# Performance work log

Hardware: AMD Instinct MI355X
Metric: run time of the kernel (lower is better)

## Reference

```python
import jax, jax.numpy as jnp
import numpy as np

B, S, D, H, DFF = 4, 2048, 1024, 8, 4096
DH = D // H  # 128
EPS = 1e-5


def layernorm(x, gamma, beta):
    mu = jnp.mean(x, axis=-1, keepdims=True)
    var = jnp.mean(jnp.square(x - mu), axis=-1, keepdims=True)
    return (x - mu) * jax.lax.rsqrt(var + EPS) * gamma + beta


def setup_inputs() -> dict:
    key = jax.random.key(0)
    ks = jax.random.split(key, 6)
    s = 0.02
    return {
        "src": jax.random.normal(ks[0], (B, S, D), jnp.float32),
        "w_qkv": jax.random.normal(ks[1], (D, 3 * D), jnp.float32) * s,
        "w_out": jax.random.normal(ks[2], (D, D), jnp.float32) * s,
        "w1": jax.random.normal(ks[3], (D, DFF), jnp.float32) * s,
        "b1": jnp.zeros((DFF,), jnp.float32),
        "w2": jax.random.normal(ks[4], (DFF, D), jnp.float32) * s,
        "b2": jnp.zeros((D,), jnp.float32),
        "g1": jnp.ones((D,), jnp.float32),
        "beta1": jnp.zeros((D,), jnp.float32),
        "g2": jnp.ones((D,), jnp.float32),
        "beta2": jnp.zeros((D,), jnp.float32),
    }


def reference(src, w_qkv, w_out, w1, b1, w2, b2, g1, beta1, g2, beta2):
    b, s, d = src.shape
    # --- RingAttention == exact causal MHA on a single device ---
    qkv = src @ w_qkv  # [b, s, 3d]
    q, k, v = jnp.split(qkv, 3, axis=-1)
    to_heads = lambda x: x.reshape(b, s, H, DH).transpose(0, 2, 1, 3)  # [b,h,s,dh]
    q, k, v = to_heads(q), to_heads(k), to_heads(v)
    scale = 1.0 / jnp.sqrt(jnp.asarray(DH, src.dtype))
    scores = jnp.einsum('bhqd,bhkd->bhqk', q, k) * scale  # [b,h,s,s]
    causal = jnp.tril(jnp.ones((s, s), bool))
    neg = jnp.asarray(jnp.finfo(src.dtype).min, src.dtype)
    scores = jnp.where(causal, scores, neg)
    attn = jax.nn.softmax(scores, axis=-1)
    o = jnp.einsum('bhqk,bhkd->bhqd', attn, v)  # [b,h,s,dh]
    o = o.transpose(0, 2, 1, 3).reshape(b, s, d) @ w_out
    # dropout layers are identity at inference
    x = layernorm(src + o, g1, beta1)
    ff = jax.nn.relu(x @ w1 + b1) @ w2 + b2
    return layernorm(x + ff, g2, beta2)
```

## Files before the change

kernel.cpp:

```cpp
#include <hip/hip_runtime.h>

typedef unsigned short u16;
typedef __attribute__((ext_vector_type(8))) short short8;
typedef __attribute__((ext_vector_type(4))) float float4v;

#define MFMA_BF16(a, b, c) __builtin_amdgcn_mfma_f32_16x16x32_bf16((a), (b), (c), 0, 0, 0)

#define B_ 4
#define S_ 2048
#define D_ 1024
#define H_ 8
#define DH_ 128
#define DFF_ 4096
#define EPS_ 1e-5f
#define ROWS_ (B_ * S_)
#define CSCALE_ 0.12751672939502f

__device__ __forceinline__ u16 f2bf(float f) {
  union { float f; unsigned u; } x; x.f = f;
  unsigned r = x.u + 0x7fffu + ((x.u >> 16) & 1u);
  return (u16)(r >> 16);
}

typedef __attribute__((address_space(1))) const unsigned int guint;
typedef __attribute__((address_space(3))) unsigned int luint;
__device__ __forceinline__ void gl2lds16(const u16* g, u16* l) {
  __builtin_amdgcn_global_load_lds((guint*)g, (luint*)l, 16, 0, 0);
}

__global__ void cast_bf16_kernel(const float* __restrict__ in, u16* __restrict__ out, int n4) {
  int i = blockIdx.x * blockDim.x + threadIdx.x;
  int stride = gridDim.x * blockDim.x;
  for (; i < n4; i += stride) {
    float4 v = ((const float4*)in)[i];
    ushort4 u;
    u.x = f2bf(v.x); u.y = f2bf(v.y); u.z = f2bf(v.z); u.w = f2bf(v.w);
    ((ushort4*)out)[i] = u;
  }
}

__global__ void transpose_cast_kernel(const float* __restrict__ in, u16* __restrict__ out,
                                      int K, int N) {
  __shared__ float t[32][33];
  int k0 = blockIdx.x * 32, n0 = blockIdx.y * 32;
  int tx = threadIdx.x & 31, ty = threadIdx.x >> 5;
  #pragma unroll
  for (int i = 0; i < 4; ++i)
    t[ty + 8 * i][tx] = in[(size_t)(k0 + ty + 8 * i) * N + n0 + tx];
  __syncthreads();
  #pragma unroll
  for (int i = 0; i < 4; ++i)
    out[(size_t)(n0 + ty + 8 * i) * K + k0 + tx] = f2bf(t[tx][ty + 8 * i]);
}

__global__ void transpose_v_kernel(const u16* __restrict__ in, u16* __restrict__ out) {
  __shared__ u16 t[32][33];
  int s0 = blockIdx.x * 32, d0 = blockIdx.y * 32, bh = blockIdx.z;
  const u16* src = in + (size_t)bh * S_ * DH_;
  u16* dst = out + (size_t)bh * DH_ * S_;
  int tx = threadIdx.x & 31, ty = threadIdx.x >> 5;
  #pragma unroll
  for (int i = 0; i < 4; ++i)
    t[ty + 8 * i][tx] = src[(size_t)(s0 + ty + 8 * i) * DH_ + d0 + tx];
  __syncthreads();
  #pragma unroll
  for (int i = 0; i < 4; ++i)
    dst[(size_t)(d0 + ty + 8 * i) * S_ + s0 + tx] = t[tx][ty + 8 * i];
}

template <int MODE>
__global__ __launch_bounds__(512, 2) void gemm256_kernel(
    const u16* __restrict__ A, const u16* __restrict__ Bt,
    const int M, const int N, const int K,
    float* __restrict__ outF, u16* __restrict__ outH, const float* __restrict__ bias,
    u16* __restrict__ qo, u16* __restrict__ ko, u16* __restrict__ vo) {
  extern __shared__ u16 smem[];
  u16* At  = smem;
  u16* Bts = smem + 2 * 256 * 64;
  const int tid = threadIdx.x;
  const int lane = tid & 63, wave = tid >> 6;
  const int quad = lane >> 4, r16 = lane & 15;
  const int halfw = wave >> 2;
  const int wn = (wave & 3) * 64;
  const int m0 = blockIdx.x * 256, n0 = blockIdx.y * 256;
  const int NT = K >> 6;

  const int rowin = wave * 8 + (lane >> 3);
  const int sc = lane & 7;
  const int shalf = rowin >> 5, srr = rowin & 31;

  const u16* Asrc[4];
  const u16* Bsrc[4];
  #pragma unroll
  for (int u = 0; u < 4; ++u) {
    const int ra = shalf * 128 + u * 32 + srr;
    Asrc[u] = A + (size_t)(m0 + ra) * K + (sc ^ (ra & 7)) * 8;
    const int rb = u * 64 + rowin;
    Bsrc[u] = Bt + (size_t)(n0 + rb) * K + (sc ^ (rb & 7)) * 8;
  }

  float4v acc[8][4];
  #pragma unroll
  for (int i = 0; i < 8; ++i)
    #pragma unroll
    for (int j = 0; j < 4; ++j) acc[i][j] = (float4v)0.0f;

#define STAGE_A(t, u) gl2lds16(Asrc[u] + (t) * 64, At  + ((t) & 1) * 16384 + (u) * 4096 + wave * 512)
#define STAGE_B(t, u) gl2lds16(Bsrc[u] + (t) * 64, Bts + ((t) & 1) * 16384 + (u) * 4096 + wave * 512)

  STAGE_B(0, 0); STAGE_B(0, 1); STAGE_B(0, 2); STAGE_B(0, 3);
  STAGE_A(0, 0); STAGE_A(0, 1); STAGE_A(0, 2); STAGE_A(0, 3);
  if (NT > 1) {
    STAGE_B(1, 0); STAGE_B(1, 1); STAGE_B(1, 2); STAGE_B(1, 3);
    STAGE_A(1, 0); STAGE_A(1, 1);
    asm volatile("s_waitcnt vmcnt(6)" ::: "memory");
  } else {
    asm volatile("s_waitcnt vmcnt(0)" ::: "memory");
  }
  __builtin_amdgcn_s_barrier();

  for (int kt = 0; kt < NT; ++kt) {
    const u16* Ab = At + (kt & 1) * 16384;
    const u16* Bb = Bts + (kt & 1) * 16384;
    short8 bfr[4][2];
    #pragma unroll
    for (int q = 0; q < 4; ++q) {
      if (q == 0) {
        #pragma unroll
        for (int j = 0; j < 4; ++j)
          #pragma unroll
          for (int s = 0; s < 2; ++s)
            bfr[j][s] = *(const short8*)(Bb + (wn + j * 16 + r16) * 64 +
                                         (((s * 4 + quad) ^ (r16 & 7)) * 8));
      }
      short8 af[2][2];
      #pragma unroll
      for (int di = 0; di < 2; ++di)
        #pragma unroll
        for (int s = 0; s < 2; ++s)
          af[di][s] = *(const short8*)(Ab + (q * 64 + halfw * 32 + di * 16 + r16) * 64 +
                                       (((s * 4 + quad) ^ (r16 & 7)) * 8));
      if (q == 0)      { if (kt + 1 < NT) { STAGE_A(kt + 1, 2); STAGE_A(kt + 1, 3); } }
      else if (q == 1) { if (kt + 2 < NT) { STAGE_B(kt + 2, 0); STAGE_B(kt + 2, 1); } }
      else if (q == 2) { if (kt + 2 < NT) { STAGE_B(kt + 2, 2); STAGE_B(kt + 2, 3); } }
      else             { if (kt + 2 < NT) { STAGE_A(kt + 2, 0); STAGE_A(kt + 2, 1); } }
      __builtin_amdgcn_s_barrier();
      asm volatile("s_waitcnt lgkmcnt(0)" ::: "memory");
      __builtin_amdgcn_s_setprio(1);
      #pragma unroll
      for (int j = 0; j < 4; ++j) {
        acc[2 * q][j]     = MFMA_BF16(af[0][0], bfr[j][0], acc[2 * q][j]);
        acc[2 * q][j]     = MFMA_BF16(af[0][1], bfr[j][1], acc[2 * q][j]);
        acc[2 * q + 1][j] = MFMA_BF16(af[1][0], bfr[j][0], acc[2 * q + 1][j]);
        acc[2 * q + 1][j] = MFMA_BF16(af[1][1], bfr[j][1], acc[2 * q + 1][j]);
      }
      __builtin_amdgcn_s_setprio(0);
      if (q == 3) {
        if (kt + 2 < NT)      { asm volatile("s_waitcnt vmcnt(6)" ::: "memory"); }
        else if (kt + 1 < NT) { asm volatile("s_waitcnt vmcnt(0)" ::: "memory"); }
      }
      __builtin_amdgcn_s_barrier();
    }
  }
#undef STAGE_A
#undef STAGE_B

  #pragma unroll
  for (int i = 0; i < 8; ++i) {
    const int rowb = m0 + halfw * 128 + i * 16 + quad * 4;
    #pragma unroll
    for (int j = 0; j < 4; ++j) {
      const int col = n0 + wn + j * 16 + r16;
      #pragma unroll
      for (int rg = 0; rg < 4; ++rg) {
        float val = acc[i][j][rg];
        const int r = rowb + rg;
        if (MODE == 2) {
          val += bias[col];
          val = fmaxf(val, 0.0f);
          outH[(size_t)r * N + col] = f2bf(val);
        } else {
          outF[(size_t)r * N + col] = val;
        }
      }
    }
  }
}

template <int MODE>
__global__ __launch_bounds__(512, 2) void gemm256x128_kernel(
    const u16* __restrict__ A, const u16* __restrict__ Bt,
    const int M, const int N, const int K,
    float* __restrict__ outF, u16* __restrict__ outH, const float* __restrict__ bias,
    u16* __restrict__ qo, u16* __restrict__ ko, u16* __restrict__ vo) {
  extern __shared__ u16 smem[];
  u16* At  = smem;
  u16* Bts = smem + 2 * 256 * 64;
  const int tid = threadIdx.x;
  const int lane = tid & 63, wave = tid >> 6;
  const int quad = lane >> 4, r16 = lane & 15;
  const int w64 = wave >> 1;
  const int wn = (wave & 1) * 64;
  const int m0 = blockIdx.x * 256, n0 = blockIdx.y * 128;
  const int NT = K >> 6;

  const int rowin = wave * 8 + (lane >> 3);
  const int sc = lane & 7;

  const u16* Asrc[4];
  const u16* Bsrc[2];
  #pragma unroll
  for (int u = 0; u < 4; ++u) {
    const int ra = ((u & 1) * 2 + (rowin >> 5)) * 64 + (u >> 1) * 32 + (rowin & 31);
    Asrc[u] = A + (size_t)(m0 + ra) * K + (sc ^ (ra & 7)) * 8;
  }
  #pragma unroll
  for (int u = 0; u < 2; ++u) {
    const int rb = u * 64 + rowin;
    Bsrc[u] = Bt + (size_t)(n0 + rb) * K + (sc ^ (rb & 7)) * 8;
  }

  float4v acc[4][4];
  #pragma unroll
  for (int i = 0; i < 4; ++i)
    #pragma unroll
    for (int j = 0; j < 4; ++j) acc[i][j] = (float4v)0.0f;

#define STAGE_A(t, u) gl2lds16(Asrc[u] + (t) * 64, At  + ((t) & 1) * 16384 + (u) * 4096 + wave * 512)
#define STAGE_B(t, u) gl2lds16(Bsrc[u] + (t) * 64, Bts + ((t) & 1) * 8192 + (u) * 4096 + wave * 512)

  STAGE_B(0, 0); STAGE_B(0, 1); STAGE_A(0, 0); STAGE_A(0, 1);
  STAGE_A(0, 2); STAGE_A(0, 3);
  STAGE_B(1, 0); STAGE_B(1, 1); STAGE_A(1, 0); STAGE_A(1, 1);
  asm volatile("s_waitcnt vmcnt(6)" ::: "memory");
  __builtin_amdgcn_s_barrier();

  for (int kt = 0; kt < NT; ++kt) {
    const u16* Ab = At + (kt & 1) * 16384;
    const u16* Bb = Bts + (kt & 1) * 8192;
    short8 bfr[4][2];
    #pragma unroll
    for (int j = 0; j < 4; ++j)
      #pragma unroll
      for (int s = 0; s < 2; ++s)
        bfr[j][s] = *(const short8*)(Bb + (wn + j * 16 + r16) * 64 +
                                     (((s * 4 + quad) ^ (r16 & 7)) * 8));
    {
      short8 af[2][2];
      #pragma unroll
      for (int di = 0; di < 2; ++di)
        #pragma unroll
        for (int s = 0; s < 2; ++s)
          af[di][s] = *(const short8*)(Ab + (w64 * 32 + di * 16 + r16) * 64 +
                                       (((s * 4 + quad) ^ (r16 & 7)) * 8));
      if (kt + 1 < NT) { STAGE_A(kt + 1, 2); STAGE_A(kt + 1, 3); }
      __builtin_amdgcn_s_barrier();
      asm volatile("s_waitcnt lgkmcnt(0)" ::: "memory");
      __builtin_amdgcn_s_setprio(1);
      #pragma unroll
      for (int j = 0; j < 4; ++j) {
        acc[0][j] = MFMA_BF16(af[0][0], bfr[j][0], acc[0][j]);
        acc[0][j] = MFMA_BF16(af[0][1], bfr[j][1], acc[0][j]);
        acc[1][j] = MFMA_BF16(af[1][0], bfr[j][0], acc[1][j]);
        acc[1][j] = MFMA_BF16(af[1][1], bfr[j][1], acc[1][j]);
      }
      __builtin_amdgcn_s_setprio(0);
      if (kt + 1 < NT) { asm volatile("s_waitcnt vmcnt(6)" ::: "memory"); }
      else             { asm volatile("s_waitcnt vmcnt(0)" ::: "memory"); }
      __builtin_amdgcn_s_barrier();
    }
    {
      short8 af[2][2];
      #pragma unroll
      for (int di = 0; di < 2; ++di)
        #pragma unroll
        for (int s = 0; s < 2; ++s)
          af[di][s] = *(const short8*)(Ab + (128 + w64 * 32 + di * 16 + r16) * 64 +
                                       (((s * 4 + quad) ^ (r16 & 7)) * 8));
      if (kt + 2 < NT) {
        STAGE_B(kt + 2, 0); STAGE_B(kt + 2, 1);
        STAGE_A(kt + 2, 0); STAGE_A(kt + 2, 1);
      }
      __builtin_amdgcn_s_barrier();
      asm volatile("s_waitcnt lgkmcnt(0)" ::: "memory");
      __builtin_amdgcn_s_setprio(1);
      #pragma unroll
      for (int j = 0; j < 4; ++j) {
        acc[2][j] = MFMA_BF16(af[0][0], bfr[j][0], acc[2][j]);
        acc[2][j] = MFMA_BF16(af[0][1], bfr[j][1], acc[2][j]);
        acc[3][j] = MFMA_BF16(af[1][0], bfr[j][0], acc[3][j]);
        acc[3][j] = MFMA_BF16(af[1][1], bfr[j][1], acc[3][j]);
      }
      __builtin_amdgcn_s_setprio(0);
      if (kt + 1 < NT) {
        if (kt + 2 < NT) { asm volatile("s_waitcnt vmcnt(6)" ::: "memory"); }
        else             { asm volatile("s_waitcnt vmcnt(2)" ::: "memory"); }
      }
      __builtin_amdgcn_s_barrier();
    }
  }
#undef STAGE_A
#undef STAGE_B

  #pragma unroll
  for (int i = 0; i < 4; ++i) {
    const int rowb = m0 + w64 * 64 + i * 16 + quad * 4;
    #pragma unroll
    for (int j = 0; j < 4; ++j) {
      const int col = n0 + wn + j * 16 + r16;
      #pragma unroll
      for (int rg = 0; rg < 4; ++rg) {
        float val = acc[i][j][rg];
        const int r = rowb + rg;
        if (MODE == 0) {
          const int part = col >> 10, cc = col & 1023;
          const int h = cc >> 7, dh = cc & 127;
          const int b = r >> 11, s = r & 2047;
          u16* dst = (part == 0) ? qo : (part == 1) ? ko : vo;
          if (part == 0) val *= CSCALE_;
          dst[((size_t)(b * H_ + h) * S_ + s) * DH_ + dh] = f2bf(val);
        } else if (MODE == 1) {
          outF[(size_t)r * N + col] = val;
        } else {
          val += bias[col];
          outF[(size_t)r * N + col] = val;
        }
      }
    }
  }
}

__global__ __launch_bounds__(256) void attn_kernel(
    const u16* __restrict__ Q, const u16* __restrict__ Kg,
    const u16* __restrict__ Vtg, u16* __restrict__ O) {
  __shared__ u16 Ks[64][136];
  __shared__ u16 Vt[128][72];
  __shared__ u16 Pw[4][16][72];
  const int tid = threadIdx.x;
  const int lane = tid & 63, wave = tid >> 6;
  const int quad = lane >> 4, r16 = lane & 15;
  const int id = blockIdx.x;
  const int bh = (id & 7) * 4 + (id >> 7);
  const int pairIdx = (id >> 3) & 15;
  const size_t base = (size_t)bh * S_ * DH_;
  const size_t vtb = (size_t)bh * DH_ * S_;
  const int b = bh >> 3, h = bh & 7;

  const u16* kg0 = Kg + base + (size_t)(tid >> 4) * DH_ + (tid & 15) * 8;
  u16* ksl = &Ks[tid >> 4][(tid & 15) * 8];
  const u16* vg0 = Vtg + vtb + (size_t)(tid >> 3) * S_ + (tid & 7) * 8;
  u16* vtl = &Vt[tid >> 3][(tid & 7) * 8];

  short8 rk[4], rv[4];
#define LOADKV(kb_)                                                        \
  do {                                                                     \
    _Pragma("unroll")                                                      \
    for (int i_ = 0; i_ < 4; ++i_)                                         \
      rk[i_] = *(const short8*)(kg0 + (size_t)((kb_) * 64 + i_ * 16) * DH_); \
    _Pragma("unroll")                                                      \
    for (int i_ = 0; i_ < 4; ++i_)                                         \
      rv[i_] = *(const short8*)(vg0 + (size_t)i_ * 32 * S_ + (kb_) * 64);  \
  } while (0)

  for (int half = 0; half < 2; ++half) {
    const int qb = (half == 0) ? pairIdx : 31 - pairIdx;
    const int qr = qb * 64 + wave * 16 + r16;

    short8 aq[4];
    #pragma unroll
    for (int ks = 0; ks < 4; ++ks)
      aq[ks] = *(const short8*)(Q + base + (size_t)qr * DH_ + ks * 32 + quad * 8);

    float4v acco[8];
    #pragma unroll
    for (int i = 0; i < 8; ++i) acco[i] = (float4v)0.0f;
    float m_q = -1e30f, l_q = 0.0f;

    LOADKV(0);

    for (int kb = 0; kb <= qb; ++kb) {
      __syncthreads();
      #pragma unroll
      for (int i = 0; i < 4; ++i) *(short8*)(ksl + i * 16 * 136) = rk[i];
      #pragma unroll
      for (int i = 0; i < 4; ++i) *(short8*)(vtl + i * 32 * 72) = rv[i];
      __syncthreads();
      if (kb < qb) LOADKV(kb + 1);

      float4v accs[4];
      #pragma unroll
      for (int t = 0; t < 4; ++t) accs[t] = (float4v)0.0f;
      #pragma unroll
      for (int ks = 0; ks < 4; ++ks) {
        #pragma unroll
        for (int t = 0; t < 4; ++t) {
          short8 ak = *(const short8*)&Ks[t * 16 + r16][ks * 32 + quad * 8];
          accs[t] = MFMA_BF16(ak, aq[ks], accs[t]);
        }
      }
      if (kb == qb) {
        #pragma unroll
        for (int t = 0; t < 4; ++t)
          #pragma unroll
          for (int rg = 0; rg < 4; ++rg) {
            int kc = kb * 64 + t * 16 + quad * 4 + rg;
            if (kc > qr) accs[t][rg] = -1e30f;
          }
      }
      float mv = accs[0][0];
      #pragma unroll
      for (int t = 0; t < 4; ++t)
        #pragma unroll
        for (int rg = 0; rg < 4; ++rg) mv = fmaxf(mv, accs[t][rg]);
      mv = fmaxf(mv, __shfl_xor(mv, 16));
      mv = fmaxf(mv, __shfl_xor(mv, 32));
      const float mnew = fmaxf(m_q, mv);
      const float alpha = __builtin_amdgcn_exp2f(m_q - mnew);
      float s0 = 0.0f;
      #pragma unroll
      for (int t = 0; t < 4; ++t)
        #pragma unroll
        for (int rg = 0; rg < 4; ++rg) {
          float p = __builtin_amdgcn_exp2f(accs[t][rg] - mnew);
          accs[t][rg] = p;
          s0 += p;
        }
      s0 += __shfl_xor(s0, 16);
      s0 += __shfl_xor(s0, 32);
      l_q = l_q * alpha + s0;
      m_q = mnew;

      #pragma unroll
      for (int t = 0; t < 4; ++t) {
        union { float f; unsigned u; } c0, c1, c2, c3;
        c0.f = accs[t][0]; c1.f = accs[t][1]; c2.f = accs[t][2]; c3.f = accs[t][3];
        uint2 pk;
        pk.x = ((c0.u + 0x8000u) >> 16) | ((c1.u + 0x8000u) & 0xffff0000u);
        pk.y = ((c2.u + 0x8000u) >> 16) | ((c3.u + 0x8000u) & 0xffff0000u);
        *(uint2*)&Pw[wave][r16][t * 16 + quad * 4] = pk;
      }
      float al[4];
      #pragma unroll
      for (int rg = 0; rg < 4; ++rg) al[rg] = __shfl(alpha, quad * 4 + rg);
      #pragma unroll
      for (int nt = 0; nt < 8; ++nt)
        #pragma unroll
        for (int rg = 0; rg < 4; ++rg) acco[nt][rg] *= al[rg];
      asm volatile("s_waitcnt lgkmcnt(0)" ::: "memory");
      #pragma unroll
      for (int ks2 = 0; ks2 < 2; ++ks2) {
        short8 ap = *(const short8*)&Pw[wave][r16][ks2 * 32 + quad * 8];
        #pragma unroll
        for (int nt = 0; nt < 8; ++nt) {
          short8 bv = *(const short8*)&Vt[nt * 16 + r16][ks2 * 32 + quad * 8];
          acco[nt] = MFMA_BF16(ap, bv, acco[nt]);
        }
      }
    }

    float lr[4];
    #pragma unroll
    for (int rg = 0; rg < 4; ++rg) lr[rg] = __shfl(l_q, quad * 4 + rg);
    const int sbase = qb * 64 + wave * 16 + quad * 4;
    #pragma unroll
    for (int nt = 0; nt < 8; ++nt)
      #pragma unroll
      for (int rg = 0; rg < 4; ++rg) {
        float val = acco[nt][rg] / lr[rg];
        O[((size_t)(b * S_ + sbase + rg)) * D_ + h * DH_ + nt * 16 + r16] = f2bf(val);
      }
  }
#undef LOADKV
}

__global__ __launch_bounds__(256) void ln_kernel(
    const float* __restrict__ a, const float* __restrict__ res,
    const float* __restrict__ g, const float* __restrict__ be,
    float* __restrict__ xf, u16* __restrict__ xb) {
  __shared__ float red[8];
  const int row = blockIdx.x, tid = threadIdx.x;
  const float4 va = ((const float4*)(a + (size_t)row * D_))[tid];
  const float4 vr = ((const float4*)(res + (size_t)row * D_))[tid];
  float4 v;
  v.x = va.x + vr.x; v.y = va.y + vr.y; v.z = va.z + vr.z; v.w = va.w + vr.w;
  float s = v.x + v.y + v.z + v.w;
  float q = v.x * v.x + v.y * v.y + v.z * v.z + v.w * v.w;
  #pragma unroll
  for (int m = 1; m < 64; m <<= 1) {
    s += __shfl_xor(s, m);
    q += __shfl_xor(q, m);
  }
  const int wave = tid >> 6, lane = tid & 63;
  if (lane == 0) { red[wave] = s; red[4 + wave] = q; }
  __syncthreads();
  s = red[0] + red[1] + red[2] + red[3];
  q = red[4] + red[5] + red[6] + red[7];
  const float mu = s * (1.0f / D_);
  const float var = q * (1.0f / D_) - mu * mu;
  const float inv = rsqrtf(var + EPS_);
  const float4 gg = ((const float4*)g)[tid];
  const float4 bb = ((const float4*)be)[tid];
  float4 y;
  y.x = (v.x - mu) * inv * gg.x + bb.x;
  y.y = (v.y - mu) * inv * gg.y + bb.y;
  y.z = (v.z - mu) * inv * gg.z + bb.z;
  y.w = (v.w - mu) * inv * gg.w + bb.w;
  ((float4*)(xf + (size_t)row * D_))[tid] = y;
  if (xb) {
    ushort4 u;
    u.x = f2bf(y.x); u.y = f2bf(y.y); u.z = f2bf(y.z); u.w = f2bf(y.w);
    ((ushort4*)(xb + (size_t)row * D_))[tid] = u;
  }
}

extern "C" void kernel_launch(void* const* d_in, const int* in_sizes, int n_in,
                              void* d_out, int out_size, void* d_ws, size_t ws_size,
                              hipStream_t stream) {
  const float* src   = (const float*)d_in[0];
  const float* w_qkv = (const float*)d_in[1];
  const float* w_out = (const float*)d_in[2];
  const float* w1    = (const float*)d_in[3];
  const float* b1    = (const float*)d_in[4];
  const float* w2    = (const float*)d_in[5];
  const float* b2    = (const float*)d_in[6];
  const float* g1    = (const float*)d_in[7];
  const float* be1   = (const float*)d_in[8];
  const float* g2    = (const float*)d_in[9];
  const float* be2   = (const float*)d_in[10];
  float* out = (float*)d_out;

  char* ws = (char*)d_ws;
  size_t off = 0;
  auto alloc = [&](size_t bytes) -> void* {
    void* p = ws + off;
    off += (bytes + 255) & ~(size_t)255;
    return p;
  };
  u16* src_bf = (u16*)alloc((size_t)ROWS_ * D_ * 2);
  u16* wqkvT  = (u16*)alloc((size_t)3 * D_ * D_ * 2);
  u16* woutT  = (u16*)alloc((size_t)D_ * D_ * 2);
  u16* w1T    = (u16*)alloc((size_t)DFF_ * D_ * 2);
  u16* w2T    = (u16*)alloc((size_t)D_ * DFF_ * 2);
  u16* qbuf   = (u16*)alloc((size_t)ROWS_ * D_ * 2);
  u16* kbuf   = (u16*)alloc((size_t)ROWS_ * D_ * 2);
  u16* vbuf   = (u16*)alloc((size_t)ROWS_ * D_ * 2);
  u16* obuf   = (u16*)alloc((size_t)ROWS_ * D_ * 2);
  u16* vT     = (u16*)alloc((size_t)ROWS_ * D_ * 2);
  float* proj = (float*)alloc((size_t)ROWS_ * D_ * 4);
  float* xf   = (float*)alloc((size_t)ROWS_ * D_ * 4);
  u16* xb     = (u16*)alloc((size_t)ROWS_ * D_ * 2);
  u16* h1     = qbuf;
  float* ff   = proj;

  const int GSMEM  = 131072;
  const int GSMEM2 = 98304;
  hipFuncSetAttribute((const void*)gemm256_kernel<2>, hipFuncAttributeMaxDynamicSharedMemorySize, GSMEM);
  hipFuncSetAttribute((const void*)gemm256x128_kernel<0>, hipFuncAttributeMaxDynamicSharedMemorySize, GSMEM2);
  hipFuncSetAttribute((const void*)gemm256x128_kernel<1>, hipFuncAttributeMaxDynamicSharedMemorySize, GSMEM2);
  hipFuncSetAttribute((const void*)gemm256x128_kernel<3>, hipFuncAttributeMaxDynamicSharedMemorySize, GSMEM2);

  cast_bf16_kernel<<<2048, 256, 0, stream>>>(src, src_bf, ROWS_ * D_ / 4);
  transpose_cast_kernel<<<dim3(D_ / 32, 3 * D_ / 32), 256, 0, stream>>>(w_qkv, wqkvT, D_, 3 * D_);
  transpose_cast_kernel<<<dim3(D_ / 32, D_ / 32), 256, 0, stream>>>(w_out, woutT, D_, D_);
  transpose_cast_kernel<<<dim3(D_ / 32, DFF_ / 32), 256, 0, stream>>>(w1, w1T, D_, DFF_);
  transpose_cast_kernel<<<dim3(DFF_ / 32, D_ / 32), 256, 0, stream>>>(w2, w2T, DFF_, D_);

  gemm256x128_kernel<0><<<dim3(ROWS_ / 256, 3 * D_ / 128), 512, GSMEM2, stream>>>(
      src_bf, wqkvT, ROWS_, 3 * D_, D_, nullptr, nullptr, nullptr, qbuf, kbuf, vbuf);
  transpose_v_kernel<<<dim3(S_ / 32, DH_ / 32, B_ * H_), 256, 0, stream>>>(vbuf, vT);
  attn_kernel<<<512, 256, 0, stream>>>(qbuf, kbuf, vT, obuf);
  gemm256x128_kernel<1><<<dim3(ROWS_ / 256, D_ / 128), 512, GSMEM2, stream>>>(
      obuf, woutT, ROWS_, D_, D_, proj, nullptr, nullptr, nullptr, nullptr, nullptr);
  ln_kernel<<<ROWS_, 256, 0, stream>>>(proj, src, g1, be1, xf, xb);
  gemm256_kernel<2><<<dim3(ROWS_ / 256, DFF_ / 256), 512, GSMEM, stream>>>(
      xb, w1T, ROWS_, DFF_, D_, nullptr, h1, b1, nullptr, nullptr, nullptr);
  gemm256x128_kernel<3><<<dim3(ROWS_ / 256, D_ / 128), 512, GSMEM2, stream>>>(
      h1, w2T, ROWS_, D_, DFF_, ff, nullptr, b2, nullptr, nullptr, nullptr);
  ln_kernel<<<ROWS_, 256, 0, stream>>>(ff, xf, g2, be2, out, nullptr);
}
```

Measured before the change: 481.3 us.

## Split-K the second FFN GEMM, unpair attention blocks, add lazy softmax rescaling

The FFN down-projection GEMM is split into two K halves across blockIdx.z. Each half writes its own fp32 partial, and the second LayerNorm sums the two partials, which raises block count for the long-K GEMM. The attention kernel drops the paired causal-block scheme and launches one block per query tile (1024 blocks), heaviest tiles first. The online softmax skips the output rescale when the running max grows by less than a threshold. The split adds an extra fp32 buffer write and read, and ff2 is placed at the start of ws, which may overlap other buffers.

```diff
diff --git a/kernel.cpp b/kernel.cpp
--- a/kernel.cpp
+++ b/kernel.cpp
@@ -190,8 +190,9 @@
 template <int MODE>
 __global__ __launch_bounds__(512, 2) void gemm256x128_kernel(
     const u16* __restrict__ A, const u16* __restrict__ Bt,
-    const int M, const int N, const int K,
-    float* __restrict__ outF, u16* __restrict__ outH, const float* __restrict__ bias,
+    const int M, const int N, const int K, const int lda,
+    float* __restrict__ outF, float* __restrict__ outF2,
+    u16* __restrict__ outH, const float* __restrict__ bias,
     u16* __restrict__ qo, u16* __restrict__ ko, u16* __restrict__ vo) {
   extern __shared__ u16 smem[];
   u16* At  = smem;
@@ -203,6 +204,7 @@
   const int wn = (wave & 1) * 64;
   const int m0 = blockIdx.x * 256, n0 = blockIdx.y * 128;
   const int NT = K >> 6;
+  const int kof = (MODE == 4) ? (int)blockIdx.z * K : 0;
 
   const int rowin = wave * 8 + (lane >> 3);
   const int sc = lane & 7;
@@ -212,12 +214,12 @@
   #pragma unroll
   for (int u = 0; u < 4; ++u) {
     const int ra = ((u & 1) * 2 + (rowin >> 5)) * 64 + (u >> 1) * 32 + (rowin & 31);
-    Asrc[u] = A + (size_t)(m0 + ra) * K + (sc ^ (ra & 7)) * 8;
+    Asrc[u] = A + (size_t)(m0 + ra) * lda + kof + (sc ^ (ra & 7)) * 8;
   }
   #pragma unroll
   for (int u = 0; u < 2; ++u) {
     const int rb = u * 64 + rowin;
-    Bsrc[u] = Bt + (size_t)(n0 + rb) * K + (sc ^ (rb & 7)) * 8;
+    Bsrc[u] = Bt + (size_t)(n0 + rb) * lda + kof + (sc ^ (rb & 7)) * 8;
   }
 
   float4v acc[4][4];
@@ -321,6 +323,10 @@
           dst[((size_t)(b * H_ + h) * S_ + s) * DH_ + dh] = f2bf(val);
         } else if (MODE == 1) {
           outF[(size_t)r * N + col] = val;
+        } else if (MODE == 4) {
+          float* dst = blockIdx.z ? outF2 : outF;
+          if (blockIdx.z == 0) val += bias[col];
+          dst[(size_t)r * N + col] = val;
         } else {
           val += bias[col];
           outF[(size_t)r * N + col] = val;
@@ -340,8 +346,8 @@
   const int lane = tid & 63, wave = tid >> 6;
   const int quad = lane >> 4, r16 = lane & 15;
   const int id = blockIdx.x;
-  const int bh = (id & 7) * 4 + (id >> 7);
-  const int pairIdx = (id >> 3) & 15;
+  const int bh = (id & 7) * 4 + ((id >> 3) & 3);
+  const int qb = 31 - (id >> 5);
   const size_t base = (size_t)bh * S_ * DH_;
   const size_t vtb = (size_t)bh * DH_ * S_;
   const int b = bh >> 3, h = bh & 7;
@@ -362,83 +368,84 @@
       rv[i_] = *(const short8*)(vg0 + (size_t)i_ * 32 * S_ + (kb_) * 64);  \
   } while (0)
 
-  for (int half = 0; half < 2; ++half) {
-    const int qb = (half == 0) ? pairIdx : 31 - pairIdx;
-    const int qr = qb * 64 + wave * 16 + r16;
-
-    short8 aq[4];
-    #pragma unroll
-    for (int ks = 0; ks < 4; ++ks)
-      aq[ks] = *(const short8*)(Q + base + (size_t)qr * DH_ + ks * 32 + quad * 8);
-
-    float4v acco[8];
-    #pragma unroll
-    for (int i = 0; i < 8; ++i) acco[i] = (float4v)0.0f;
-    float m_q = -1e30f, l_q = 0.0f;
-
-    LOADKV(0);
-
-    for (int kb = 0; kb <= qb; ++kb) {
-      __syncthreads();
-      #pragma unroll
-      for (int i = 0; i < 4; ++i) *(short8*)(ksl + i * 16 * 136) = rk[i];
-      #pragma unroll
-      for (int i = 0; i < 4; ++i) *(short8*)(vtl + i * 32 * 72) = rv[i];
-      __syncthreads();
-      if (kb < qb) LOADKV(kb + 1);
-
-      float4v accs[4];
-      #pragma unroll
-      for (int t = 0; t < 4; ++t) accs[t] = (float4v)0.0f;
-      #pragma unroll
-      for (int ks = 0; ks < 4; ++ks) {
-        #pragma unroll
-        for (int t = 0; t < 4; ++t) {
-          short8 ak = *(const short8*)&Ks[t * 16 + r16][ks * 32 + quad * 8];
-          accs[t] = MFMA_BF16(ak, aq[ks], accs[t]);
-        }
-      }
-      if (kb == qb) {
-        #pragma unroll
-        for (int t = 0; t < 4; ++t)
-          #pragma unroll
-          for (int rg = 0; rg < 4; ++rg) {
-            int kc = kb * 64 + t * 16 + quad * 4 + rg;
-            if (kc > qr) accs[t][rg] = -1e30f;
-          }
-      }
-      float mv = accs[0][0];
-      #pragma unroll
-      for (int t = 0; t < 4; ++t)
-        #pragma unroll
-        for (int rg = 0; rg < 4; ++rg) mv = fmaxf(mv, accs[t][rg]);
-      mv = fmaxf(mv, __shfl_xor(mv, 16));
-      mv = fmaxf(mv, __shfl_xor(mv, 32));
-      const float mnew = fmaxf(m_q, mv);
-      const float alpha = __builtin_amdgcn_exp2f(m_q - mnew);
-      float s0 = 0.0f;
+  const int qr = qb * 64 + wave * 16 + r16;
+
+  short8 aq[4];
+  #pragma unroll
+  for (int ks = 0; ks < 4; ++ks)
+    aq[ks] = *(const short8*)(Q + base + (size_t)qr * DH_ + ks * 32 + quad * 8);
+
+  float4v acco[8];
+  #pragma unroll
+  for (int i = 0; i < 8; ++i) acco[i] = (float4v)0.0f;
+  float m_q = -1e30f, l_q = 0.0f;
+
+  LOADKV(0);
+
+  for (int kb = 0; kb <= qb; ++kb) {
+    __syncthreads();
+    #pragma unroll
+    for (int i = 0; i < 4; ++i) *(short8*)(ksl + i * 16 * 136) = rk[i];
+    #pragma unroll
+    for (int i = 0; i < 4; ++i) *(short8*)(vtl + i * 32 * 72) = rv[i];
+    __syncthreads();
+    if (kb < qb) LOADKV(kb + 1);
+
+    float4v accs[4];
+    #pragma unroll
+    for (int t = 0; t < 4; ++t) accs[t] = (float4v)0.0f;
+    #pragma unroll
+    for (int ks = 0; ks < 4; ++ks) {
+      #pragma unroll
+      for (int t = 0; t < 4; ++t) {
+        short8 ak = *(const short8*)&Ks[t * 16 + r16][ks * 32 + quad * 8];
+        accs[t] = MFMA_BF16(ak, aq[ks], accs[t]);
+      }
+    }
+    if (kb == qb) {
       #pragma unroll
       for (int t = 0; t < 4; ++t)
         #pragma unroll
         for (int rg = 0; rg < 4; ++rg) {
-          float p = __builtin_amdgcn_exp2f(accs[t][rg] - mnew);
-          accs[t][rg] = p;
-          s0 += p;
+          int kc = kb * 64 + t * 16 + quad * 4 + rg;
+          if (kc > qr) accs[t][rg] = -1e30f;
         }
-      s0 += __shfl_xor(s0, 16);
-      s0 += __shfl_xor(s0, 32);
-      l_q = l_q * alpha + s0;
-      m_q = mnew;
-
-      #pragma unroll
-      for (int t = 0; t < 4; ++t) {
-        union { float f; unsigned u; } c0, c1, c2, c3;
-        c0.f = accs[t][0]; c1.f = accs[t][1]; c2.f = accs[t][2]; c3.f = accs[t][3];
-        uint2 pk;
-        pk.x = ((c0.u + 0x8000u) >> 16) | ((c1.u + 0x8000u) & 0xffff0000u);
-        pk.y = ((c2.u + 0x8000u) >> 16) | ((c3.u + 0x8000u) & 0xffff0000u);
-        *(uint2*)&Pw[wave][r16][t * 16 + quad * 4] = pk;
-      }
+    }
+    float mv = accs[0][0];
+    #pragma unroll
+    for (int t = 0; t < 4; ++t)
+      #pragma unroll
+      for (int rg = 0; rg < 4; ++rg) mv = fmaxf(mv, accs[t][rg]);
+    mv = fmaxf(mv, __shfl_xor(mv, 16));
+    mv = fmaxf(mv, __shfl_xor(mv, 32));
+    const bool nore = __all(mv <= m_q + 8.0f) != 0;
+    const float mnew = nore ? m_q : fmaxf(m_q, mv);
+    float alpha = 1.0f;
+    if (!nore) alpha = __builtin_amdgcn_exp2f(m_q - mnew);
+    float s0 = 0.0f;
+    #pragma unroll
+    for (int t = 0; t < 4; ++t)
+      #pragma unroll
+      for (int rg = 0; rg < 4; ++rg) {
+        float p = __builtin_amdgcn_exp2f(accs[t][rg] - mnew);
+        accs[t][rg] = p;
+        s0 += p;
+      }
+    s0 += __shfl_xor(s0, 16);
+    s0 += __shfl_xor(s0, 32);
+    l_q = nore ? (l_q + s0) : (l_q * alpha + s0);
+    m_q = mnew;
+
+    #pragma unroll
+    for (int t = 0; t < 4; ++t) {
+      union { float f; unsigned u; } c0, c1, c2, c3;
+      c0.f = accs[t][0]; c1.f = accs[t][1]; c2.f = accs[t][2]; c3.f = accs[t][3];
+      uint2 pk;
+      pk.x = ((c0.u + 0x8000u) >> 16) | ((c1.u + 0x8000u) & 0xffff0000u);
+      pk.y = ((c2.u + 0x8000u) >> 16) | ((c3.u + 0x8000u) & 0xffff0000u);
+      *(uint2*)&Pw[wave][r16][t * 16 + quad * 4] = pk;
+    }
+    if (!nore) {
       float al[4];
       #pragma unroll
       for (int rg = 0; rg < 4; ++rg) al[rg] = __shfl(alpha, quad * 4 + rg);
@@ -446,35 +453,36 @@
       for (int nt = 0; nt < 8; ++nt)
         #pragma unroll
         for (int rg = 0; rg < 4; ++rg) acco[nt][rg] *= al[rg];
-      asm volatile("s_waitcnt lgkmcnt(0)" ::: "memory");
-      #pragma unroll
-      for (int ks2 = 0; ks2 < 2; ++ks2) {
-        short8 ap = *(const short8*)&Pw[wave][r16][ks2 * 32 + quad * 8];
-        #pragma unroll
-        for (int nt = 0; nt < 8; ++nt) {
-          short8 bv = *(const short8*)&Vt[nt * 16 + r16][ks2 * 32 + quad * 8];
-          acco[nt] = MFMA_BF16(ap, bv, acco[nt]);
-        }
-      }
-    }
-
-    float lr[4];
-    #pragma unroll
-    for (int rg = 0; rg < 4; ++rg) lr[rg] = __shfl(l_q, quad * 4 + rg);
-    const int sbase = qb * 64 + wave * 16 + quad * 4;
-    #pragma unroll
-    for (int nt = 0; nt < 8; ++nt)
-      #pragma unroll
-      for (int rg = 0; rg < 4; ++rg) {
-        float val = acco[nt][rg] / lr[rg];
-        O[((size_t)(b * S_ + sbase + rg)) * D_ + h * DH_ + nt * 16 + r16] = f2bf(val);
-      }
-  }
+    }
+    asm volatile("s_waitcnt lgkmcnt(0)" ::: "memory");
+    #pragma unroll
+    for (int ks2 = 0; ks2 < 2; ++ks2) {
+      short8 ap = *(const short8*)&Pw[wave][r16][ks2 * 32 + quad * 8];
+      #pragma unroll
+      for (int nt = 0; nt < 8; ++nt) {
+        short8 bv = *(const short8*)&Vt[nt * 16 + r16][ks2 * 32 + quad * 8];
+        acco[nt] = MFMA_BF16(ap, bv, acco[nt]);
+      }
+    }
+  }
+
+  float lr[4];
+  #pragma unroll
+  for (int rg = 0; rg < 4; ++rg) lr[rg] = __shfl(l_q, quad * 4 + rg);
+  const int sbase = qb * 64 + wave * 16 + quad * 4;
+  #pragma unroll
+  for (int nt = 0; nt < 8; ++nt)
+    #pragma unroll
+    for (int rg = 0; rg < 4; ++rg) {
+      float val = acco[nt][rg] / lr[rg];
+      O[((size_t)(b * S_ + sbase + rg)) * D_ + h * DH_ + nt * 16 + r16] = f2bf(val);
+    }
 #undef LOADKV
 }
 
 __global__ __launch_bounds__(256) void ln_kernel(
-    const float* __restrict__ a, const float* __restrict__ res,
+    const float* __restrict__ a, const float* __restrict__ a2,
+    const float* __restrict__ res,
     const float* __restrict__ g, const float* __restrict__ be,
     float* __restrict__ xf, u16* __restrict__ xb) {
   __shared__ float red[8];
@@ -483,6 +491,10 @@
   const float4 vr = ((const float4*)(res + (size_t)row * D_))[tid];
   float4 v;
   v.x = va.x + vr.x; v.y = va.y + vr.y; v.z = va.z + vr.z; v.w = va.w + vr.w;
+  if (a2) {
+    const float4 v2 = ((const float4*)(a2 + (size_t)row * D_))[tid];
+    v.x += v2.x; v.y += v2.y; v.z += v2.z; v.w += v2.w;
+  }
   float s = v.x + v.y + v.z + v.w;
   float q = v.x * v.x + v.y * v.y + v.z * v.z + v.w * v.w;
   #pragma unroll
@@ -551,13 +563,14 @@
   u16* xb     = (u16*)alloc((size_t)ROWS_ * D_ * 2);
   u16* h1     = qbuf;
   float* ff   = proj;
+  float* ff2  = (float*)ws;
 
   const int GSMEM  = 131072;
   const int GSMEM2 = 98304;
   hipFuncSetAttribute((const void*)gemm256_kernel<2>, hipFuncAttributeMaxDynamicSharedMemorySize, GSMEM);
   hipFuncSetAttribute((const void*)gemm256x128_kernel<0>, hipFuncAttributeMaxDynamicSharedMemorySize, GSMEM2);
   hipFuncSetAttribute((const void*)gemm256x128_kernel<1>, hipFuncAttributeMaxDynamicSharedMemorySize, GSMEM2);
-  hipFuncSetAttribute((const void*)gemm256x128_kernel<3>, hipFuncAttributeMaxDynamicSharedMemorySize, GSMEM2);
+  hipFuncSetAttribute((const void*)gemm256x128_kernel<4>, hipFuncAttributeMaxDynamicSharedMemorySize, GSMEM2);
 
   cast_bf16_kernel<<<2048, 256, 0, stream>>>(src, src_bf, ROWS_ * D_ / 4);
   transpose_cast_kernel<<<dim3(D_ / 32, 3 * D_ / 32), 256, 0, stream>>>(w_qkv, wqkvT, D_, 3 * D_);
@@ -566,15 +579,15 @@
   transpose_cast_kernel<<<dim3(DFF_ / 32, D_ / 32), 256, 0, stream>>>(w2, w2T, DFF_, D_);
 
   gemm256x128_kernel<0><<<dim3(ROWS_ / 256, 3 * D_ / 128), 512, GSMEM2, stream>>>(
-      src_bf, wqkvT, ROWS_, 3 * D_, D_, nullptr, nullptr, nullptr, qbuf, kbuf, vbuf);
+      src_bf, wqkvT, ROWS_, 3 * D_, D_, D_, nullptr, nullptr, nullptr, nullptr, qbuf, kbuf, vbuf);
   transpose_v_kernel<<<dim3(S_ / 32, DH_ / 32, B_ * H_), 256, 0, stream>>>(vbuf, vT);
-  attn_kernel<<<512, 256, 0, stream>>>(qbuf, kbuf, vT, obuf);
+  attn_kernel<<<1024, 256, 0, stream>>>(qbuf, kbuf, vT, obuf);
   gemm256x128_kernel<1><<<dim3(ROWS_ / 256, D_ / 128), 512, GSMEM2, stream>>>(
-      obuf, woutT, ROWS_, D_, D_, proj, nullptr, nullptr, nullptr, nullptr, nullptr);
-  ln_kernel<<<ROWS_, 256, 0, stream>>>(proj, src, g1, be1, xf, xb);
+      obuf, woutT, ROWS_, D_, D_, D_, proj, nullptr, nullptr, nullptr, nullptr, nullptr, nullptr);
+  ln_kernel<<<ROWS_, 256, 0, stream>>>(proj, nullptr, src, g1, be1, xf, xb);
   gemm256_kernel<2><<<dim3(ROWS_ / 256, DFF_ / 256), 512, GSMEM, stream>>>(
       xb, w1T, ROWS_, DFF_, D_, nullptr, h1, b1, nullptr, nullptr, nullptr);
-  gemm256x128_kernel<3><<<dim3(ROWS_ / 256, D_ / 128), 512, GSMEM2, stream>>>(
-      h1, w2T, ROWS_, D_, DFF_, ff, nullptr, b2, nullptr, nullptr, nullptr);
-  ln_kernel<<<ROWS_, 256, 0, stream>>>(ff, xf, g2, be2, out, nullptr);
-}
+  gemm256x128_kernel<4><<<dim3(ROWS_ / 256, D_ / 128, 2), 512, GSMEM2, stream>>>(
+      h1, w2T, ROWS_, D_, DFF_ / 2, DFF_, ff, ff2, nullptr, b2, nullptr, nullptr, nullptr);
+  ln_kernel<<<ROWS_, 256, 0, stream>>>(ff, ff2, xf, g2, be2, out, nullptr);
+}
```

Result: slower. 502.2 us (+4.3%).
